# Performance work log

Measured on AMD Instinct MI355X. Metric: run time of the kernel, lower is better.

## Reference

```python
import jax, jax.numpy as jnp
import numpy as np

B, C, H, W = 4, 64, 128, 128
NP = 9        # num_param (N offset points per pixel)
OUTC = 128
STRIDE = 1
EPS = 1e-5    # BatchNorm eps


def _conv(x, w, b=None, stride=1):
    out = jax.lax.conv_general_dilated(
        x, w, (stride, stride), 'SAME',
        dimension_numbers=('NCHW', 'OIHW', 'NCHW'))
    if b is not None:
        out = out + b[None, :, None, None]
    return out


def setup_inputs() -> dict:
    key = jax.random.key(0)
    ks = jax.random.split(key, 6)
    s = lambda k, sh, sc: jax.random.normal(k, sh, jnp.float32) * sc
    return dict(
        x=s(ks[0], (B, C, H, W), 1.0),
        p_w=s(ks[1], (2 * NP, C, 3, 3), 0.02),   # offset conv (3x3, pad 1)
        p_b=s(ks[2], (2 * NP,), 0.02),
        conv_w=s(ks[3], (OUTC, C, 1, 1), 0.05),  # final 1x1 conv, no bias
        bn_gamma=jnp.ones((OUTC,), jnp.float32),
        bn_beta=jnp.zeros((OUTC,), jnp.float32),
        attn_w=s(ks[4], (1, C, 1, 1), 0.05),
        attn_b=s(ks[5], (1,), 0.05),
    )


def _forward(x, p_w, p_b, conv_w, bn_gamma, bn_beta, attn_w, attn_b):
    N = NP
    # density attention (computed as in source; adaptive re-parameterization skipped)
    density = jax.nn.sigmoid(_conv(x, attn_w, attn_b))  # noqa: F841

    # learned offsets: [B, 2N, H, W] (first N channels = row/x, last N = col/y)
    offset = _conv(x, p_w, p_b, stride=STRIDE)

    # p_n: base kernel grid offsets (row-major 3x3 -> values 0..2)
    base_int = int(round(np.sqrt(NP)))
    row_number = NP // base_int
    ii, jj = np.meshgrid(np.arange(row_number), np.arange(base_int), indexing='ij')
    p_n = jnp.asarray(np.concatenate([ii.ravel(), jj.ravel()]).astype(np.float32))  # [2N]

    # p_0: per-pixel base coordinates
    p0x = jnp.broadcast_to(jnp.arange(H, dtype=jnp.float32)[:, None] * STRIDE, (H, W))
    p0y = jnp.broadcast_to(jnp.arange(W, dtype=jnp.float32)[None, :] * STRIDE, (H, W))
    p_0 = jnp.concatenate([jnp.broadcast_to(p0x, (N, H, W)),
                           jnp.broadcast_to(p0y, (N, H, W))], axis=0)  # [2N,H,W]

    # sampling locations p: [B, H, W, 2N]
    p = (offset + p_n[None, :, None, None] + p_0[None]).transpose(0, 2, 3, 1)

    q_lt = jax.lax.stop_gradient(jnp.floor(p))   # detached, as in source
    q_rb = q_lt + 1.0
    px, py = p[..., :N], p[..., N:]
    ltx, lty = q_lt[..., :N], q_lt[..., N:]
    rbx, rby = q_rb[..., :N], q_rb[..., N:]

    # bilinear weights
    g_lt = (1 + (ltx - px)) * (1 + (lty - py))
    g_rb = (1 - (rbx - px)) * (1 - (rby - py))
    g_lb = (1 + (ltx - px)) * (1 - (rby - py))
    g_rt = (1 - (rbx - px)) * (1 + (lty - py))

    HW = H * W
    x_flat = x.reshape(B, C, HW)

    def gather(qx, qy):
        idx = jnp.clip((qx * W + qy).astype(jnp.int32), 0, HW - 1)  # [B,H,W,N]
        idx = idx.reshape(B, -1)
        out = jax.vmap(lambda xf, ix: xf[:, ix])(x_flat, idx)       # [B,C,H*W*N]
        return out.reshape(B, C, H, W, N)

    x_off = (g_lt[:, None] * gather(ltx, lty)
             + g_rb[:, None] * gather(rbx, rby)
             + g_lb[:, None] * gather(ltx, rby)
             + g_rt[:, None] * gather(rbx, lty))    # [B,C,H,W,N]

    # rearrange 'b c h w n -> b c (h n) w'
    x_off = x_off.transpose(0, 1, 2, 4, 3).reshape(B, C, H * N, W)

    # 1x1 conv (no bias) + BatchNorm2d (training-mode batch stats) + SiLU
    y = _conv(x_off, conv_w)
    mean = y.mean(axis=(0, 2, 3))
    var = y.var(axis=(0, 2, 3))  # biased, as torch BN uses for normalization
    y = (y - mean[None, :, None, None]) * jax.lax.rsqrt(var[None, :, None, None] + EPS)
    y = y * bn_gamma[None, :, None, None] + bn_beta[None, :, None, None]
    return jax.nn.silu(y)


def reference(x, p_w, p_b, conv_w, bn_gamma, bn_beta, attn_w, attn_b):
    return _forward(x, p_w, p_b, conv_w, bn_gamma, bn_beta, attn_w, attn_b)
```

## Files before the change

### kernel.cpp

```cpp
#include <hip/hip_runtime.h>

#define CIN   64
#define NOUT  128
#define IMH   128
#define IMW   128
#define NPTS  9
#define NB    4
#define HW    (IMH*IMW)
#define ROWS  (IMH*NPTS)
#define CHS   (ROWS*IMW)
#define TOTAL ((size_t)NB*NOUT*CHS)

typedef float f32x4 __attribute__((ext_vector_type(4)));
typedef unsigned short ushort_t;

__device__ __forceinline__ ushort_t f2bf(float f) {
    union { float f; unsigned u; } a; a.f = f;
    unsigned r = a.u + 0x7FFFu + ((a.u >> 16) & 1u);
    return (ushort_t)(r >> 16);
}

__device__ __forceinline__ void cvt8(uint4 v, float* f) {
    f[0] = __uint_as_float(v.x << 16); f[1] = __uint_as_float(v.x & 0xFFFF0000u);
    f[2] = __uint_as_float(v.y << 16); f[3] = __uint_as_float(v.y & 0xFFFF0000u);
    f[4] = __uint_as_float(v.z << 16); f[5] = __uint_as_float(v.z & 0xFFFF0000u);
    f[6] = __uint_as_float(v.w << 16); f[7] = __uint_as_float(v.w & 0xFFFF0000u);
}

__global__ __launch_bounds__(256) void k_offset(const float* __restrict__ x,
                                                const float* __restrict__ pw,
                                                const float* __restrict__ pb,
                                                float* __restrict__ off,
                                                float* __restrict__ stats0) {
    __shared__ float wl[576 * 20];
    __shared__ float red[3 * 64 * 19];

    int tid = threadIdx.x;
    if (blockIdx.x == 0) stats0[tid] = 0.f;

    for (int t = tid; t < 18 * 576; t += 256) {
        int k = t / 576, cj = t % 576;
        wl[cj * 20 + k] = pw[t];
    }
    __syncthreads();

    int cg = tid >> 6;
    int lp = tid & 63;
    int gid = blockIdx.x * 64 + lp;
    int b = gid >> 14;
    int hw = gid & 16383;
    int h = hw >> 7;
    int w = hw & 127;

    float acc[18];
#pragma unroll
    for (int k = 0; k < 18; ++k) acc[k] = (cg == 0) ? pb[k] : 0.f;

    const float* xb = x + (size_t)b * CIN * HW;
    int c0 = cg * 16;
    for (int c = c0; c < c0 + 16; ++c) {
        const float* xc = xb + c * HW;
#pragma unroll
        for (int dh = 0; dh < 3; ++dh) {
            int hh = h + dh - 1;
            if ((unsigned)hh >= 128u) continue;
#pragma unroll
            for (int dw = 0; dw < 3; ++dw) {
                int ww = w + dw - 1;
                if ((unsigned)ww >= 128u) continue;
                float xv = xc[hh * IMW + ww];
                const float* wr = &wl[(c * 9 + dh * 3 + dw) * 20];
                float wv[18];
                *(float4*)&wv[0]  = *(const float4*)(wr);
                *(float4*)&wv[4]  = *(const float4*)(wr + 4);
                *(float4*)&wv[8]  = *(const float4*)(wr + 8);
                *(float4*)&wv[12] = *(const float4*)(wr + 12);
                *(float2*)&wv[16] = *(const float2*)(wr + 16);
#pragma unroll
                for (int k = 0; k < 18; ++k) acc[k] += wv[k] * xv;
            }
        }
    }

    if (cg > 0) {
        float* rp = &red[((cg - 1) * 64 + lp) * 19];
#pragma unroll
        for (int k = 0; k < 18; ++k) rp[k] = acc[k];
    }
    __syncthreads();
    if (cg == 0) {
#pragma unroll
        for (int k = 0; k < 18; ++k)
            acc[k] += red[(0 * 64 + lp) * 19 + k] + red[(64 + lp) * 19 + k] + red[(128 + lp) * 19 + k];
        float* ob = off + (size_t)b * 18 * HW + hw;
#pragma unroll
        for (int k = 0; k < 18; ++k) ob[k * HW] = acc[k];
    }
}

__global__ __launch_bounds__(256) void k_z(const float* __restrict__ x,
                                           const float* __restrict__ cw,
                                           ushort_t* __restrict__ z) {
    __shared__ float xs[64 * 128];
    __shared__ float wsm[64 * 128];
    int tid = threadIdx.x;
    int b   = blockIdx.x >> 7;
    int hw0 = (blockIdx.x & 127) << 7;

    const float* xb = x + (size_t)b * CIN * HW + hw0;
#pragma unroll
    for (int i = 0; i < 32; ++i) {
        int t = tid + i * 256;
        int c = t >> 7, l = t & 127;
        xs[t] = xb[c * HW + l];
    }
#pragma unroll
    for (int i = 0; i < 32; ++i) {
        int t = tid + i * 256;
        int oc = t & 127, c = t >> 7;
        wsm[c * 128 + oc] = cw[oc * 64 + c];
    }
    __syncthreads();

    int hw4  = (tid & 31) << 2;
    int oc16 = (tid >> 5) << 4;

    float acc[4][16];
#pragma unroll
    for (int j = 0; j < 4; ++j)
#pragma unroll
        for (int k = 0; k < 16; ++k) acc[j][k] = 0.f;

    for (int c = 0; c < 64; ++c) {
        float4 xv = *(const float4*)&xs[c * 128 + hw4];
        float xq[4] = {xv.x, xv.y, xv.z, xv.w};
        float wv[16];
        const float4* wrow = (const float4*)&wsm[c * 128 + oc16];
#pragma unroll
        for (int m = 0; m < 4; ++m) ((float4*)wv)[m] = wrow[m];
#pragma unroll
        for (int j = 0; j < 4; ++j)
#pragma unroll
            for (int k = 0; k < 16; ++k) acc[j][k] += xq[j] * wv[k];
    }

#pragma unroll
    for (int j = 0; j < 4; ++j) {
        ushort_t* zr = z + ((size_t)b * HW + hw0 + hw4 + j) * NOUT + oc16;
        union { ushort_t u[16]; uint4 q[2]; } pk;
#pragma unroll
        for (int k = 0; k < 16; ++k) pk.u[k] = f2bf(acc[j][k]);
        *(uint4*)zr       = pk.q[0];
        *(uint4*)(zr + 8) = pk.q[1];
    }
}

__device__ __forceinline__ void bilin_setup(const float* __restrict__ off,
                                            int b, int h, int n, int w,
                                            float4& g, int4& id) {
    const float* ob = off + ((size_t)b * 18 + n) * HW + h * IMW + w;
    float ox = ob[0];
    float oy = ob[9 * HW];
    float px = ox + (float)(n / 3) + (float)h;
    float py = oy + (float)(n % 3) + (float)w;
    float fX = floorf(px), fY = floorf(py);
    float fx = px - fX, fy = py - fY;
    int X = (int)fX, Y = (int)fY;
    g.x = (1.f - fx) * (1.f - fy);
    g.y = fx * fy;
    g.z = (1.f - fx) * fy;
    g.w = fx * (1.f - fy);
    id.x = min(max(X * IMW + Y, 0), HW - 1) * NOUT;
    id.y = min(max((X + 1) * IMW + (Y + 1), 0), HW - 1) * NOUT;
    id.z = min(max(X * IMW + (Y + 1), 0), HW - 1) * NOUT;
    id.w = min(max((X + 1) * IMW + Y, 0), HW - 1) * NOUT;
}

__device__ __forceinline__ int swz_block() {
    return (blockIdx.x & 7) * 576 + (blockIdx.x >> 3);
}

__global__ __launch_bounds__(256) void k_sum(const float* __restrict__ off,
                                             const ushort_t* __restrict__ z,
                                             float* __restrict__ gsum,
                                             float* __restrict__ gsq) {
    int logical = swz_block();
    int n  = logical % 9;
    int t2 = logical / 9;
    int h  = t2 & 127;
    int b  = t2 >> 7;

    __shared__ float4 gS[128];
    __shared__ int4   iS[128];
    __shared__ float  lsum[128];
    __shared__ float  lsq[128];

    int tid = threadIdx.x;
    if (tid < 128) {
        lsum[tid] = 0.f; lsq[tid] = 0.f;
        float4 g; int4 id;
        bilin_setup(off, b, h, n, tid, g, id);
        gS[tid] = g; iS[tid] = id;
    }
    __syncthreads();

    int g16 = tid >> 4;
    int c8  = (tid & 15) << 3;
    const ushort_t* zb = z + (size_t)b * HW * NOUT + c8;

    float s[8], q[8];
#pragma unroll
    for (int k = 0; k < 8; ++k) { s[k] = 0.f; q[k] = 0.f; }

    uint4 plt, prb, plb, prt;
    {
        int4 id = iS[g16];
        plt = *(const uint4*)(zb + id.x);
        prb = *(const uint4*)(zb + id.y);
        plb = *(const uint4*)(zb + id.z);
        prt = *(const uint4*)(zb + id.w);
    }
#pragma unroll
    for (int wi = 0; wi < 8; ++wi) {
        uint4 nlt, nrb, nlb, nrt;
        if (wi < 7) {
            int4 idn = iS[((wi + 1) << 4) + g16];
            nlt = *(const uint4*)(zb + idn.x);
            nrb = *(const uint4*)(zb + idn.y);
            nlb = *(const uint4*)(zb + idn.z);
            nrt = *(const uint4*)(zb + idn.w);
        }
        float4 g = gS[(wi << 4) + g16];
        float flt[8], frb[8], flb[8], frt[8];
        cvt8(plt, flt); cvt8(prb, frb); cvt8(plb, flb); cvt8(prt, frt);
#pragma unroll
        for (int k = 0; k < 8; ++k) {
            float a = g.x * flt[k] + g.y * frb[k] + g.z * flb[k] + g.w * frt[k];
            s[k] += a; q[k] += a * a;
        }
        plt = nlt; prb = nrb; plb = nlb; prt = nrt;
    }

#pragma unroll
    for (int k = 0; k < 8; ++k) {
        s[k] += __shfl_xor(s[k], 16, 64); s[k] += __shfl_xor(s[k], 32, 64);
        q[k] += __shfl_xor(q[k], 16, 64); q[k] += __shfl_xor(q[k], 32, 64);
    }
    if (((tid >> 4) & 3) == 0) {
#pragma unroll
        for (int k = 0; k < 8; ++k) {
            atomicAdd(&lsum[c8 + k], s[k]);
            atomicAdd(&lsq[c8 + k],  q[k]);
        }
    }
    __syncthreads();
    if (tid < 128)       atomicAdd(&gsum[tid],      lsum[tid]);
    else                 atomicAdd(&gsq[tid - 128], lsq[tid - 128]);
}

__device__ __forceinline__ void proc8(const uint4* C, float4 g,
                                      const float* sc, const float* sh,
                                      float* __restrict__ dst) {
    float flt[8], frb[8], flb[8], frt[8];
    cvt8(C[0], flt); cvt8(C[1], frb); cvt8(C[2], flb); cvt8(C[3], frt);
    float o[8];
#pragma unroll
    for (int k = 0; k < 8; ++k) {
        float t = (g.x * flt[k] + g.y * frb[k] + g.z * flb[k] + g.w * frt[k]) * sc[k] + sh[k];
        o[k] = t / (1.f + __expf(-t));
    }
    *(float4*)dst       = *(float4*)&o[0];
    *(float4*)(dst + 4) = *(float4*)&o[4];
}

__global__ __launch_bounds__(256) void k_apply(const float* __restrict__ off,
                                               const ushort_t* __restrict__ z,
                                               const float* __restrict__ gsum,
                                               const float* __restrict__ gsq,
                                               const float* __restrict__ gamma,
                                               const float* __restrict__ beta,
                                               float* __restrict__ out) {
    int logical = swz_block();
    int n  = logical % 9;
    int t2 = logical / 9;
    int h  = t2 & 127;
    int b  = t2 >> 7;

    __shared__ float4 gS[128];
    __shared__ int4   iS[128];
    __shared__ float  scS[128];
    __shared__ float  shS[128];
    __shared__ float  ybuf[2][32 * 133];

    int tid = threadIdx.x;
    if (tid < 128) {
        const float cnt = (float)(NB * ROWS * IMW);
        float m  = gsum[tid] / cnt;
        float vv = gsq[tid] / cnt - m * m;
        float inv = rsqrtf(fmaxf(vv, 0.f) + 1e-5f);
        float sc = inv * gamma[tid];
        scS[tid] = sc;
        shS[tid] = beta[tid] - m * sc;
        float4 g; int4 id;
        bilin_setup(off, b, h, n, tid, g, id);
        gS[tid] = g; iS[tid] = id;
    }
    __syncthreads();

    int g16 = tid >> 4;
    int c8  = (tid & 15) << 3;
    float scv[8], shv[8];
    *(float4*)&scv[0] = *(const float4*)&scS[c8];
    *(float4*)&scv[4] = *(const float4*)&scS[c8 + 4];
    *(float4*)&shv[0] = *(const float4*)&shS[c8];
    *(float4*)&shv[4] = *(const float4*)&shS[c8 + 4];

    const ushort_t* zb = z + (size_t)b * HW * NOUT + c8;
    int r = h * 9 + n;
    float* outr = out + (size_t)b * NOUT * CHS + (size_t)r * IMW;

    uint4 A[8];
#define STAGE(wb) { int4 _i0 = iS[(wb) + g16]; int4 _i1 = iS[(wb) + 16 + g16]; \
    A[0] = *(const uint4*)(zb + _i0.x); A[1] = *(const uint4*)(zb + _i0.y); \
    A[2] = *(const uint4*)(zb + _i0.z); A[3] = *(const uint4*)(zb + _i0.w); \
    A[4] = *(const uint4*)(zb + _i1.x); A[5] = *(const uint4*)(zb + _i1.y); \
    A[6] = *(const uint4*)(zb + _i1.z); A[7] = *(const uint4*)(zb + _i1.w); }
#define PROC(wb, bi) { \
    proc8(&A[0], gS[(wb) + g16],      scv, shv, &ybuf[bi][g16 * 133 + c8]); \
    proc8(&A[4], gS[(wb) + 16 + g16], scv, shv, &ybuf[bi][(16 + g16) * 133 + c8]); }

    STAGE(0);
    PROC(0, 0);
    __syncthreads();

#pragma unroll
    for (int chunk = 0; chunk < 4; ++chunk) {
        const int cur = chunk & 1;
        const int nxt = cur ^ 1;
        int w0 = chunk << 5;

        if (chunk < 3) STAGE(w0 + 32);

#pragma unroll
        for (int i = 0; i < 4; ++i) {
            int task = (i << 8) + tid;
            int oc   = task >> 3;
            int w4   = (task & 7) << 2;
            f32x4 v;
            v.x = ybuf[cur][(w4 + 0) * 133 + oc];
            v.y = ybuf[cur][(w4 + 1) * 133 + oc];
            v.z = ybuf[cur][(w4 + 2) * 133 + oc];
            v.w = ybuf[cur][(w4 + 3) * 133 + oc];
            __builtin_nontemporal_store(v, (f32x4*)(outr + (size_t)oc * CHS + w0 + w4));
        }

        if (chunk < 3) PROC(w0 + 32, nxt);
        __syncthreads();
    }
#undef STAGE
#undef PROC
}

extern "C" void kernel_launch(void* const* d_in, const int* in_sizes, int n_in,
                              void* d_out, int out_size, void* d_ws, size_t ws_size,
                              hipStream_t stream) {
    const float* x     = (const float*)d_in[0];
    const float* pw    = (const float*)d_in[1];
    const float* pb    = (const float*)d_in[2];
    const float* cw    = (const float*)d_in[3];
    const float* gamma = (const float*)d_in[4];
    const float* beta  = (const float*)d_in[5];

    float* out = (float*)d_out;
    float* ws  = (float*)d_ws;

    float*    off  = ws;
    ushort_t* z    = (ushort_t*)(off + (size_t)NB * 18 * HW);
    float*    gsum = (float*)(z + (size_t)NB * HW * NOUT);
    float*    gsq  = gsum + NOUT;

    hipLaunchKernelGGL(k_offset, dim3(1024), dim3(256), 0, stream, x, pw, pb, off, gsum);
    hipLaunchKernelGGL(k_z,      dim3(512),  dim3(256), 0, stream, x, cw, z);
    hipLaunchKernelGGL(k_sum,    dim3(4608), dim3(256), 0, stream, off, z, gsum, gsq);
    hipLaunchKernelGGL(k_apply,  dim3(4608), dim3(256), 0, stream, off, z, gsum, gsq, gamma, beta, out);
}
```

Before: 303.4 us.

## Merge offset and z kernels; single-buffer apply stage for higher occupancy

Fuses the offset-conv and 1x1 z projection kernels into one launch that splits blocks 2:1 between the two jobs, removing a launch and letting them overlap on the device. In the apply kernel, the double-buffered gather/transpose pipeline is replaced by a single shared buffer with a sync per chunk, and a minimum-occupancy launch bound is added. BN scale/shift setup moves to the otherwise idle upper half of threads. This trades prefetch overlap for more resident waves.

```diff
diff --git a/kernel.cpp b/kernel.cpp
--- a/kernel.cpp
+++ b/kernel.cpp
@@ -27,131 +27,134 @@
     f[6] = __uint_as_float(v.w << 16); f[7] = __uint_as_float(v.w & 0xFFFF0000u);
 }
 
-__global__ __launch_bounds__(256) void k_offset(const float* __restrict__ x,
-                                                const float* __restrict__ pw,
-                                                const float* __restrict__ pb,
-                                                float* __restrict__ off,
-                                                float* __restrict__ stats0) {
-    __shared__ float wl[576 * 20];
-    __shared__ float red[3 * 64 * 19];
-
+__global__ __launch_bounds__(256) void k_pre(const float* __restrict__ x,
+                                             const float* __restrict__ pw,
+                                             const float* __restrict__ pb,
+                                             const float* __restrict__ cw,
+                                             float* __restrict__ off,
+                                             ushort_t* __restrict__ z,
+                                             float* __restrict__ stats0) {
+    __shared__ float smem[16384];
+    int bi = blockIdx.x;
+    int g  = bi / 3, r = bi % 3;
     int tid = threadIdx.x;
-    if (blockIdx.x == 0) stats0[tid] = 0.f;
-
-    for (int t = tid; t < 18 * 576; t += 256) {
-        int k = t / 576, cj = t % 576;
-        wl[cj * 20 + k] = pw[t];
-    }
-    __syncthreads();
-
-    int cg = tid >> 6;
-    int lp = tid & 63;
-    int gid = blockIdx.x * 64 + lp;
-    int b = gid >> 14;
-    int hw = gid & 16383;
-    int h = hw >> 7;
-    int w = hw & 127;
-
-    float acc[18];
-#pragma unroll
-    for (int k = 0; k < 18; ++k) acc[k] = (cg == 0) ? pb[k] : 0.f;
-
-    const float* xb = x + (size_t)b * CIN * HW;
-    int c0 = cg * 16;
-    for (int c = c0; c < c0 + 16; ++c) {
-        const float* xc = xb + c * HW;
-#pragma unroll
-        for (int dh = 0; dh < 3; ++dh) {
-            int hh = h + dh - 1;
-            if ((unsigned)hh >= 128u) continue;
-#pragma unroll
-            for (int dw = 0; dw < 3; ++dw) {
-                int ww = w + dw - 1;
-                if ((unsigned)ww >= 128u) continue;
-                float xv = xc[hh * IMW + ww];
-                const float* wr = &wl[(c * 9 + dh * 3 + dw) * 20];
-                float wv[18];
-                *(float4*)&wv[0]  = *(const float4*)(wr);
-                *(float4*)&wv[4]  = *(const float4*)(wr + 4);
-                *(float4*)&wv[8]  = *(const float4*)(wr + 8);
-                *(float4*)&wv[12] = *(const float4*)(wr + 12);
-                *(float2*)&wv[16] = *(const float2*)(wr + 16);
-#pragma unroll
-                for (int k = 0; k < 18; ++k) acc[k] += wv[k] * xv;
+
+    if (r == 2) {
+        if (g == 0) stats0[tid] = 0.f;
+        float* xs  = smem;
+        float* wsm = smem + 8192;
+        int b   = g >> 7;
+        int hw0 = (g & 127) << 7;
+
+        const float* xb = x + (size_t)b * CIN * HW + hw0;
+#pragma unroll
+        for (int i = 0; i < 32; ++i) {
+            int t = tid + i * 256;
+            int c = t >> 7, l = t & 127;
+            xs[t] = xb[c * HW + l];
+        }
+#pragma unroll
+        for (int i = 0; i < 32; ++i) {
+            int t = tid + i * 256;
+            int oc = t & 127, c = t >> 7;
+            wsm[c * 128 + oc] = cw[oc * 64 + c];
+        }
+        __syncthreads();
+
+        int hw4  = (tid & 31) << 2;
+        int oc16 = (tid >> 5) << 4;
+
+        float acc[4][16];
+#pragma unroll
+        for (int j = 0; j < 4; ++j)
+#pragma unroll
+            for (int k = 0; k < 16; ++k) acc[j][k] = 0.f;
+
+        for (int c = 0; c < 64; ++c) {
+            float4 xv = *(const float4*)&xs[c * 128 + hw4];
+            float xq[4] = {xv.x, xv.y, xv.z, xv.w};
+            float wv[16];
+            const float4* wrow = (const float4*)&wsm[c * 128 + oc16];
+#pragma unroll
+            for (int m = 0; m < 4; ++m) ((float4*)wv)[m] = wrow[m];
+#pragma unroll
+            for (int j = 0; j < 4; ++j)
+#pragma unroll
+                for (int k = 0; k < 16; ++k) acc[j][k] += xq[j] * wv[k];
+        }
+
+#pragma unroll
+        for (int j = 0; j < 4; ++j) {
+            ushort_t* zr = z + ((size_t)b * HW + hw0 + hw4 + j) * NOUT + oc16;
+            union { ushort_t u[16]; uint4 q[2]; } pk;
+#pragma unroll
+            for (int k = 0; k < 16; ++k) pk.u[k] = f2bf(acc[j][k]);
+            *(uint4*)zr       = pk.q[0];
+            *(uint4*)(zr + 8) = pk.q[1];
+        }
+    } else {
+        int ob = g * 2 + r;
+        float* wl  = smem;
+        float* red = smem + 11520;
+
+        for (int t = tid; t < 18 * 576; t += 256) {
+            int k = t / 576, cj = t % 576;
+            wl[cj * 20 + k] = pw[t];
+        }
+        __syncthreads();
+
+        int cg = tid >> 6;
+        int lp = tid & 63;
+        int gid = ob * 64 + lp;
+        int b = gid >> 14;
+        int hw = gid & 16383;
+        int h = hw >> 7;
+        int w = hw & 127;
+
+        float acc[18];
+#pragma unroll
+        for (int k = 0; k < 18; ++k) acc[k] = (cg == 0) ? pb[k] : 0.f;
+
+        const float* xb = x + (size_t)b * CIN * HW;
+        int c0 = cg * 16;
+        for (int c = c0; c < c0 + 16; ++c) {
+            const float* xc = xb + c * HW;
+#pragma unroll
+            for (int dh = 0; dh < 3; ++dh) {
+                int hh = h + dh - 1;
+                if ((unsigned)hh >= 128u) continue;
+#pragma unroll
+                for (int dw = 0; dw < 3; ++dw) {
+                    int ww = w + dw - 1;
+                    if ((unsigned)ww >= 128u) continue;
+                    float xv = xc[hh * IMW + ww];
+                    const float* wr = &wl[(c * 9 + dh * 3 + dw) * 20];
+                    float wv[18];
+                    *(float4*)&wv[0]  = *(const float4*)(wr);
+                    *(float4*)&wv[4]  = *(const float4*)(wr + 4);
+                    *(float4*)&wv[8]  = *(const float4*)(wr + 8);
+                    *(float4*)&wv[12] = *(const float4*)(wr + 12);
+                    *(float2*)&wv[16] = *(const float2*)(wr + 16);
+#pragma unroll
+                    for (int k = 0; k < 18; ++k) acc[k] += wv[k] * xv;
+                }
             }
         }
-    }
-
-    if (cg > 0) {
-        float* rp = &red[((cg - 1) * 64 + lp) * 19];
-#pragma unroll
-        for (int k = 0; k < 18; ++k) rp[k] = acc[k];
-    }
-    __syncthreads();
-    if (cg == 0) {
-#pragma unroll
-        for (int k = 0; k < 18; ++k)
-            acc[k] += red[(0 * 64 + lp) * 19 + k] + red[(64 + lp) * 19 + k] + red[(128 + lp) * 19 + k];
-        float* ob = off + (size_t)b * 18 * HW + hw;
-#pragma unroll
-        for (int k = 0; k < 18; ++k) ob[k * HW] = acc[k];
-    }
-}
-
-__global__ __launch_bounds__(256) void k_z(const float* __restrict__ x,
-                                           const float* __restrict__ cw,
-                                           ushort_t* __restrict__ z) {
-    __shared__ float xs[64 * 128];
-    __shared__ float wsm[64 * 128];
-    int tid = threadIdx.x;
-    int b   = blockIdx.x >> 7;
-    int hw0 = (blockIdx.x & 127) << 7;
-
-    const float* xb = x + (size_t)b * CIN * HW + hw0;
-#pragma unroll
-    for (int i = 0; i < 32; ++i) {
-        int t = tid + i * 256;
-        int c = t >> 7, l = t & 127;
-        xs[t] = xb[c * HW + l];
-    }
-#pragma unroll
-    for (int i = 0; i < 32; ++i) {
-        int t = tid + i * 256;
-        int oc = t & 127, c = t >> 7;
-        wsm[c * 128 + oc] = cw[oc * 64 + c];
-    }
-    __syncthreads();
-
-    int hw4  = (tid & 31) << 2;
-    int oc16 = (tid >> 5) << 4;
-
-    float acc[4][16];
-#pragma unroll
-    for (int j = 0; j < 4; ++j)
-#pragma unroll
-        for (int k = 0; k < 16; ++k) acc[j][k] = 0.f;
-
-    for (int c = 0; c < 64; ++c) {
-        float4 xv = *(const float4*)&xs[c * 128 + hw4];
-        float xq[4] = {xv.x, xv.y, xv.z, xv.w};
-        float wv[16];
-        const float4* wrow = (const float4*)&wsm[c * 128 + oc16];
-#pragma unroll
-        for (int m = 0; m < 4; ++m) ((float4*)wv)[m] = wrow[m];
-#pragma unroll
-        for (int j = 0; j < 4; ++j)
-#pragma unroll
-            for (int k = 0; k < 16; ++k) acc[j][k] += xq[j] * wv[k];
-    }
-
-#pragma unroll
-    for (int j = 0; j < 4; ++j) {
-        ushort_t* zr = z + ((size_t)b * HW + hw0 + hw4 + j) * NOUT + oc16;
-        union { ushort_t u[16]; uint4 q[2]; } pk;
-#pragma unroll
-        for (int k = 0; k < 16; ++k) pk.u[k] = f2bf(acc[j][k]);
-        *(uint4*)zr       = pk.q[0];
-        *(uint4*)(zr + 8) = pk.q[1];
+
+        if (cg > 0) {
+            float* rp = &red[((cg - 1) * 64 + lp) * 19];
+#pragma unroll
+            for (int k = 0; k < 18; ++k) rp[k] = acc[k];
+        }
+        __syncthreads();
+        if (cg == 0) {
+#pragma unroll
+            for (int k = 0; k < 18; ++k)
+                acc[k] += red[(0 * 64 + lp) * 19 + k] + red[(64 + lp) * 19 + k] + red[(128 + lp) * 19 + k];
+            float* obp = off + (size_t)b * 18 * HW + hw;
+#pragma unroll
+            for (int k = 0; k < 18; ++k) obp[k * HW] = acc[k];
+        }
     }
 }
 
@@ -258,11 +261,11 @@
     else                 atomicAdd(&gsq[tid - 128], lsq[tid - 128]);
 }
 
-__device__ __forceinline__ void proc8(const uint4* C, float4 g,
+__device__ __forceinline__ void proc8(uint4 C0, uint4 C1, uint4 C2, uint4 C3, float4 g,
                                       const float* sc, const float* sh,
                                       float* __restrict__ dst) {
     float flt[8], frb[8], flb[8], frt[8];
-    cvt8(C[0], flt); cvt8(C[1], frb); cvt8(C[2], flb); cvt8(C[3], frt);
+    cvt8(C0, flt); cvt8(C1, frb); cvt8(C2, flb); cvt8(C3, frt);
     float o[8];
 #pragma unroll
     for (int k = 0; k < 8; ++k) {
@@ -273,13 +276,13 @@
     *(float4*)(dst + 4) = *(float4*)&o[4];
 }
 
-__global__ __launch_bounds__(256) void k_apply(const float* __restrict__ off,
-                                               const ushort_t* __restrict__ z,
-                                               const float* __restrict__ gsum,
-                                               const float* __restrict__ gsq,
-                                               const float* __restrict__ gamma,
-                                               const float* __restrict__ beta,
-                                               float* __restrict__ out) {
+__global__ __launch_bounds__(256, 5) void k_apply(const float* __restrict__ off,
+                                                  const ushort_t* __restrict__ z,
+                                                  const float* __restrict__ gsum,
+                                                  const float* __restrict__ gsq,
+                                                  const float* __restrict__ gamma,
+                                                  const float* __restrict__ beta,
+                                                  float* __restrict__ out) {
     int logical = swz_block();
     int n  = logical % 9;
     int t2 = logical / 9;
@@ -290,20 +293,22 @@
     __shared__ int4   iS[128];
     __shared__ float  scS[128];
     __shared__ float  shS[128];
-    __shared__ float  ybuf[2][32 * 133];
+    __shared__ float  ybuf[32 * 133];
 
     int tid = threadIdx.x;
     if (tid < 128) {
-        const float cnt = (float)(NB * ROWS * IMW);
-        float m  = gsum[tid] / cnt;
-        float vv = gsq[tid] / cnt - m * m;
-        float inv = rsqrtf(fmaxf(vv, 0.f) + 1e-5f);
-        float sc = inv * gamma[tid];
-        scS[tid] = sc;
-        shS[tid] = beta[tid] - m * sc;
         float4 g; int4 id;
         bilin_setup(off, b, h, n, tid, g, id);
         gS[tid] = g; iS[tid] = id;
+    } else {
+        int c = tid - 128;
+        const float cnt = (float)(NB * ROWS * IMW);
+        float m  = gsum[c] / cnt;
+        float vv = gsq[c] / cnt - m * m;
+        float inv = rsqrtf(fmaxf(vv, 0.f) + 1e-5f);
+        float sc = inv * gamma[c];
+        scS[c] = sc;
+        shS[c] = beta[c] - m * sc;
     }
     __syncthreads();
 
@@ -319,46 +324,38 @@
     int r = h * 9 + n;
     float* outr = out + (size_t)b * NOUT * CHS + (size_t)r * IMW;
 
-    uint4 A[8];
-#define STAGE(wb) { int4 _i0 = iS[(wb) + g16]; int4 _i1 = iS[(wb) + 16 + g16]; \
-    A[0] = *(const uint4*)(zb + _i0.x); A[1] = *(const uint4*)(zb + _i0.y); \
-    A[2] = *(const uint4*)(zb + _i0.z); A[3] = *(const uint4*)(zb + _i0.w); \
-    A[4] = *(const uint4*)(zb + _i1.x); A[5] = *(const uint4*)(zb + _i1.y); \
-    A[6] = *(const uint4*)(zb + _i1.z); A[7] = *(const uint4*)(zb + _i1.w); }
-#define PROC(wb, bi) { \
-    proc8(&A[0], gS[(wb) + g16],      scv, shv, &ybuf[bi][g16 * 133 + c8]); \
-    proc8(&A[4], gS[(wb) + 16 + g16], scv, shv, &ybuf[bi][(16 + g16) * 133 + c8]); }
-
-    STAGE(0);
-    PROC(0, 0);
-    __syncthreads();
-
 #pragma unroll
     for (int chunk = 0; chunk < 4; ++chunk) {
-        const int cur = chunk & 1;
-        const int nxt = cur ^ 1;
         int w0 = chunk << 5;
-
-        if (chunk < 3) STAGE(w0 + 32);
-
+        {
+            int4 i0 = iS[w0 + g16];
+            int4 i1 = iS[w0 + 16 + g16];
+            uint4 a0 = *(const uint4*)(zb + i0.x);
+            uint4 a1 = *(const uint4*)(zb + i0.y);
+            uint4 a2 = *(const uint4*)(zb + i0.z);
+            uint4 a3 = *(const uint4*)(zb + i0.w);
+            uint4 b0 = *(const uint4*)(zb + i1.x);
+            uint4 b1 = *(const uint4*)(zb + i1.y);
+            uint4 b2 = *(const uint4*)(zb + i1.z);
+            uint4 b3 = *(const uint4*)(zb + i1.w);
+            proc8(a0, a1, a2, a3, gS[w0 + g16],      scv, shv, &ybuf[g16 * 133 + c8]);
+            proc8(b0, b1, b2, b3, gS[w0 + 16 + g16], scv, shv, &ybuf[(16 + g16) * 133 + c8]);
+        }
+        __syncthreads();
 #pragma unroll
         for (int i = 0; i < 4; ++i) {
             int task = (i << 8) + tid;
             int oc   = task >> 3;
             int w4   = (task & 7) << 2;
             f32x4 v;
-            v.x = ybuf[cur][(w4 + 0) * 133 + oc];
-            v.y = ybuf[cur][(w4 + 1) * 133 + oc];
-            v.z = ybuf[cur][(w4 + 2) * 133 + oc];
-            v.w = ybuf[cur][(w4 + 3) * 133 + oc];
+            v.x = ybuf[(w4 + 0) * 133 + oc];
+            v.y = ybuf[(w4 + 1) * 133 + oc];
+            v.z = ybuf[(w4 + 2) * 133 + oc];
+            v.w = ybuf[(w4 + 3) * 133 + oc];
             __builtin_nontemporal_store(v, (f32x4*)(outr + (size_t)oc * CHS + w0 + w4));
         }
-
-        if (chunk < 3) PROC(w0 + 32, nxt);
-        __syncthreads();
-    }
-#undef STAGE
-#undef PROC
+        __syncthreads();
+    }
 }
 
 extern "C" void kernel_launch(void* const* d_in, const int* in_sizes, int n_in,
@@ -379,8 +376,7 @@
     float*    gsum = (float*)(z + (size_t)NB * HW * NOUT);
     float*    gsq  = gsum + NOUT;
 
-    hipLaunchKernelGGL(k_offset, dim3(1024), dim3(256), 0, stream, x, pw, pb, off, gsum);
-    hipLaunchKernelGGL(k_z,      dim3(512),  dim3(256), 0, stream, x, cw, z);
-    hipLaunchKernelGGL(k_sum,    dim3(4608), dim3(256), 0, stream, off, z, gsum, gsq);
-    hipLaunchKernelGGL(k_apply,  dim3(4608), dim3(256), 0, stream, off, z, gsum, gsq, gamma, beta, out);
-}
+    hipLaunchKernelGGL(k_pre,   dim3(1536), dim3(256), 0, stream, x, pw, pb, cw, off, z, gsum);
+    hipLaunchKernelGGL(k_sum,   dim3(4608), dim3(256), 0, stream, off, z, gsum, gsq);
+    hipLaunchKernelGGL(k_apply, dim3(4608), dim3(256), 0, stream, off, z, gsum, gsq, gamma, beta, out);
+}
```

Measured after the change: 312.8 us. 1.03x slower.

## Materialize bilinear-gathered activations in bf16 instead of regathering in apply pass

Applied to the files above, without the earlier changes.

The stats pass now writes the bilinearly interpolated 1x1-conv outputs to a bf16 workspace buffer, and the apply pass reads that buffer linearly instead of recomputing offsets and doing four random gathers per point. This removes the duplicate gather and bilinear setup from the second pass. In exchange it adds a write and a read of a buffer about 75 MB in size, drops the software prefetch in the gather loop, and rounds the interpolated values to bf16 before normalization.

```diff
diff --git a/kernel.cpp b/kernel.cpp
--- a/kernel.cpp
+++ b/kernel.cpp
@@ -9,9 +9,9 @@
 #define HW    (IMH*IMW)
 #define ROWS  (IMH*NPTS)
 #define CHS   (ROWS*IMW)
-#define TOTAL ((size_t)NB*NOUT*CHS)
-
-typedef float f32x4 __attribute__((ext_vector_type(4)));
+
+typedef float    f32x4 __attribute__((ext_vector_type(4)));
+typedef unsigned u32x4 __attribute__((ext_vector_type(4)));
 typedef unsigned short ushort_t;
 
 __device__ __forceinline__ ushort_t f2bf(float f) {
@@ -20,7 +20,7 @@
     return (ushort_t)(r >> 16);
 }
 
-__device__ __forceinline__ void cvt8(uint4 v, float* f) {
+__device__ __forceinline__ void cvt8(u32x4 v, float* f) {
     f[0] = __uint_as_float(v.x << 16); f[1] = __uint_as_float(v.x & 0xFFFF0000u);
     f[2] = __uint_as_float(v.y << 16); f[3] = __uint_as_float(v.y & 0xFFFF0000u);
     f[4] = __uint_as_float(v.z << 16); f[5] = __uint_as_float(v.z & 0xFFFF0000u);
@@ -180,10 +180,11 @@
     return (blockIdx.x & 7) * 576 + (blockIdx.x >> 3);
 }
 
-__global__ __launch_bounds__(256) void k_sum(const float* __restrict__ off,
-                                             const ushort_t* __restrict__ z,
-                                             float* __restrict__ gsum,
-                                             float* __restrict__ gsq) {
+__global__ __launch_bounds__(256) void k_gather(const float* __restrict__ off,
+                                                const ushort_t* __restrict__ z,
+                                                ushort_t* __restrict__ abuf,
+                                                float* __restrict__ gsum,
+                                                float* __restrict__ gsq) {
     int logical = swz_block();
     int n  = logical % 9;
     int t2 = logical / 9;
@@ -207,38 +208,34 @@
     int g16 = tid >> 4;
     int c8  = (tid & 15) << 3;
     const ushort_t* zb = z + (size_t)b * HW * NOUT + c8;
+    int r = h * 9 + n;
+    ushort_t* ab = abuf + ((size_t)(b * ROWS + r)) * IMW * NOUT + c8;
 
     float s[8], q[8];
 #pragma unroll
     for (int k = 0; k < 8; ++k) { s[k] = 0.f; q[k] = 0.f; }
 
-    uint4 plt, prb, plb, prt;
-    {
-        int4 id = iS[g16];
-        plt = *(const uint4*)(zb + id.x);
-        prb = *(const uint4*)(zb + id.y);
-        plb = *(const uint4*)(zb + id.z);
-        prt = *(const uint4*)(zb + id.w);
-    }
 #pragma unroll
     for (int wi = 0; wi < 8; ++wi) {
-        uint4 nlt, nrb, nlb, nrt;
-        if (wi < 7) {
-            int4 idn = iS[((wi + 1) << 4) + g16];
-            nlt = *(const uint4*)(zb + idn.x);
-            nrb = *(const uint4*)(zb + idn.y);
-            nlb = *(const uint4*)(zb + idn.z);
-            nrt = *(const uint4*)(zb + idn.w);
-        }
-        float4 g = gS[(wi << 4) + g16];
+        int w = (wi << 4) + g16;
+        int4  id = iS[w];
+        float4 g = gS[w];
+        u32x4 vlt = *(const u32x4*)(zb + id.x);
+        u32x4 vrb = *(const u32x4*)(zb + id.y);
+        u32x4 vlb = *(const u32x4*)(zb + id.z);
+        u32x4 vrt = *(const u32x4*)(zb + id.w);
         float flt[8], frb[8], flb[8], frt[8];
-        cvt8(plt, flt); cvt8(prb, frb); cvt8(plb, flb); cvt8(prt, frt);
+        cvt8(vlt, flt); cvt8(vrb, frb); cvt8(vlb, flb); cvt8(vrt, frt);
+        float a[8];
 #pragma unroll
         for (int k = 0; k < 8; ++k) {
-            float a = g.x * flt[k] + g.y * frb[k] + g.z * flb[k] + g.w * frt[k];
-            s[k] += a; q[k] += a * a;
-        }
-        plt = nlt; prb = nrb; plb = nlb; prt = nrt;
+            a[k] = g.x * flt[k] + g.y * frb[k] + g.z * flb[k] + g.w * frt[k];
+            s[k] += a[k]; q[k] += a[k] * a[k];
+        }
+        union { ushort_t u[8]; u32x4 v; } pk;
+#pragma unroll
+        for (int k = 0; k < 8; ++k) pk.u[k] = f2bf(a[k]);
+        __builtin_nontemporal_store(pk.v, (u32x4*)(ab + (size_t)w * NOUT));
     }
 
 #pragma unroll
@@ -258,39 +255,19 @@
     else                 atomicAdd(&gsq[tid - 128], lsq[tid - 128]);
 }
 
-__device__ __forceinline__ void proc8(const uint4* C, float4 g,
-                                      const float* sc, const float* sh,
-                                      float* __restrict__ dst) {
-    float flt[8], frb[8], flb[8], frt[8];
-    cvt8(C[0], flt); cvt8(C[1], frb); cvt8(C[2], flb); cvt8(C[3], frt);
-    float o[8];
-#pragma unroll
-    for (int k = 0; k < 8; ++k) {
-        float t = (g.x * flt[k] + g.y * frb[k] + g.z * flb[k] + g.w * frt[k]) * sc[k] + sh[k];
-        o[k] = t / (1.f + __expf(-t));
-    }
-    *(float4*)dst       = *(float4*)&o[0];
-    *(float4*)(dst + 4) = *(float4*)&o[4];
-}
-
-__global__ __launch_bounds__(256) void k_apply(const float* __restrict__ off,
-                                               const ushort_t* __restrict__ z,
+__global__ __launch_bounds__(256) void k_apply(const ushort_t* __restrict__ abuf,
                                                const float* __restrict__ gsum,
                                                const float* __restrict__ gsq,
                                                const float* __restrict__ gamma,
                                                const float* __restrict__ beta,
                                                float* __restrict__ out) {
-    int logical = swz_block();
-    int n  = logical % 9;
-    int t2 = logical / 9;
-    int h  = t2 & 127;
-    int b  = t2 >> 7;
-
-    __shared__ float4 gS[128];
-    __shared__ int4   iS[128];
-    __shared__ float  scS[128];
-    __shared__ float  shS[128];
-    __shared__ float  ybuf[2][32 * 133];
+    int bi = blockIdx.x;
+    int b  = bi / ROWS;
+    int r  = bi % ROWS;
+
+    __shared__ float scS[128];
+    __shared__ float shS[128];
+    __shared__ float ybuf[32 * 133];
 
     int tid = threadIdx.x;
     if (tid < 128) {
@@ -301,9 +278,6 @@
         float sc = inv * gamma[tid];
         scS[tid] = sc;
         shS[tid] = beta[tid] - m * sc;
-        float4 g; int4 id;
-        bilin_setup(off, b, h, n, tid, g, id);
-        gS[tid] = g; iS[tid] = id;
     }
     __syncthreads();
 
@@ -315,50 +289,47 @@
     *(float4*)&shv[0] = *(const float4*)&shS[c8];
     *(float4*)&shv[4] = *(const float4*)&shS[c8 + 4];
 
-    const ushort_t* zb = z + (size_t)b * HW * NOUT + c8;
-    int r = h * 9 + n;
+    const ushort_t* ar = abuf + ((size_t)(b * ROWS + r)) * IMW * NOUT + c8;
     float* outr = out + (size_t)b * NOUT * CHS + (size_t)r * IMW;
 
-    uint4 A[8];
-#define STAGE(wb) { int4 _i0 = iS[(wb) + g16]; int4 _i1 = iS[(wb) + 16 + g16]; \
-    A[0] = *(const uint4*)(zb + _i0.x); A[1] = *(const uint4*)(zb + _i0.y); \
-    A[2] = *(const uint4*)(zb + _i0.z); A[3] = *(const uint4*)(zb + _i0.w); \
-    A[4] = *(const uint4*)(zb + _i1.x); A[5] = *(const uint4*)(zb + _i1.y); \
-    A[6] = *(const uint4*)(zb + _i1.z); A[7] = *(const uint4*)(zb + _i1.w); }
-#define PROC(wb, bi) { \
-    proc8(&A[0], gS[(wb) + g16],      scv, shv, &ybuf[bi][g16 * 133 + c8]); \
-    proc8(&A[4], gS[(wb) + 16 + g16], scv, shv, &ybuf[bi][(16 + g16) * 133 + c8]); }
-
-    STAGE(0);
-    PROC(0, 0);
-    __syncthreads();
-
 #pragma unroll
     for (int chunk = 0; chunk < 4; ++chunk) {
-        const int cur = chunk & 1;
-        const int nxt = cur ^ 1;
         int w0 = chunk << 5;
-
-        if (chunk < 3) STAGE(w0 + 32);
-
+        {
+            u32x4 va = *(const u32x4*)(ar + (size_t)(w0 + g16) * NOUT);
+            u32x4 vb = *(const u32x4*)(ar + (size_t)(w0 + 16 + g16) * NOUT);
+            float fa[8], fb[8];
+            cvt8(va, fa); cvt8(vb, fb);
+            float oa[8], ob[8];
+#pragma unroll
+            for (int k = 0; k < 8; ++k) {
+                float t = fa[k] * scv[k] + shv[k];
+                oa[k] = t / (1.f + __expf(-t));
+                float u = fb[k] * scv[k] + shv[k];
+                ob[k] = u / (1.f + __expf(-u));
+            }
+            float* d0 = &ybuf[g16 * 133 + c8];
+            float* d1 = &ybuf[(16 + g16) * 133 + c8];
+            *(float4*)d0       = *(float4*)&oa[0];
+            *(float4*)(d0 + 4) = *(float4*)&oa[4];
+            *(float4*)d1       = *(float4*)&ob[0];
+            *(float4*)(d1 + 4) = *(float4*)&ob[4];
+        }
+        __syncthreads();
 #pragma unroll
         for (int i = 0; i < 4; ++i) {
             int task = (i << 8) + tid;
             int oc   = task >> 3;
             int w4   = (task & 7) << 2;
             f32x4 v;
-            v.x = ybuf[cur][(w4 + 0) * 133 + oc];
-            v.y = ybuf[cur][(w4 + 1) * 133 + oc];
-            v.z = ybuf[cur][(w4 + 2) * 133 + oc];
-            v.w = ybuf[cur][(w4 + 3) * 133 + oc];
+            v.x = ybuf[(w4 + 0) * 133 + oc];
+            v.y = ybuf[(w4 + 1) * 133 + oc];
+            v.z = ybuf[(w4 + 2) * 133 + oc];
+            v.w = ybuf[(w4 + 3) * 133 + oc];
             __builtin_nontemporal_store(v, (f32x4*)(outr + (size_t)oc * CHS + w0 + w4));
         }
-
-        if (chunk < 3) PROC(w0 + 32, nxt);
         __syncthreads();
     }
-#undef STAGE
-#undef PROC
 }
 
 extern "C" void kernel_launch(void* const* d_in, const int* in_sizes, int n_in,
@@ -376,11 +347,12 @@
 
     float*    off  = ws;
     ushort_t* z    = (ushort_t*)(off + (size_t)NB * 18 * HW);
-    float*    gsum = (float*)(z + (size_t)NB * HW * NOUT);
+    ushort_t* abuf = z + (size_t)NB * HW * NOUT;
+    float*    gsum = (float*)(abuf + (size_t)NB * ROWS * IMW * NOUT);
     float*    gsq  = gsum + NOUT;
 
     hipLaunchKernelGGL(k_offset, dim3(1024), dim3(256), 0, stream, x, pw, pb, off, gsum);
     hipLaunchKernelGGL(k_z,      dim3(512),  dim3(256), 0, stream, x, cw, z);
-    hipLaunchKernelGGL(k_sum,    dim3(4608), dim3(256), 0, stream, off, z, gsum, gsq);
-    hipLaunchKernelGGL(k_apply,  dim3(4608), dim3(256), 0, stream, off, z, gsum, gsq, gamma, beta, out);
-}
+    hipLaunchKernelGGL(k_gather, dim3(4608), dim3(256), 0, stream, off, z, abuf, gsum, gsq);
+    hipLaunchKernelGGL(k_apply,  dim3(4608), dim3(256), 0, stream, abuf, gsum, gsq, gamma, beta, out);
+}
```

Result: slower. 337.6 us (+11.2%).
